# Kernel tuning notes

Hardware: AMD Instinct MI355X
Metric: run time of the kernel (lower is better)

## Reference

```python
import jax, jax.numpy as jnp
import numpy as np

N, D, E, T, R, KMEM, DE = 50000, 128, 800000, 400000, 1, 32, 16
EPS = 1e-5
BETA_MAX = 5.0
GRAD_CLIP = 1.0
STATE_CLIP = 10.0
STEP = 0.1
DAMP = 0.9999  # update_damping=1.0 clamped to 1-1e-4 as in __init__


def segment_logsumexp(s, idx, n):
    # numerically-stable per-segment logsumexp; empty segments contribute 0
    m = jax.ops.segment_max(s, idx, num_segments=n)
    ms = jnp.where(jnp.isfinite(m), m, 0.0)
    z = jax.ops.segment_sum(jnp.exp(s - ms[idx]), idx, num_segments=n)
    return jnp.where(z > 0, jnp.log(jnp.maximum(z, 1e-30)) + ms, 0.0)


def setup_inputs() -> dict:
    key = jax.random.key(0)
    ks = jax.random.split(key, 24)
    inv1 = jnp.log(jnp.expm1(jnp.float32(1.0)))  # _inv_softplus(1.0)
    xav = 0.5 * np.sqrt(2.0 / (2 * D))  # xavier_uniform gain=0.5 ~ std
    inp = {
        'X': jax.random.normal(ks[0], (N, D), jnp.float32),
        'edge_attr': jax.random.normal(ks[1], (E, DE), jnp.float32),
        'ln_gamma': jnp.ones((D,), jnp.float32),
        'ln_beta': jnp.zeros((D,), jnp.float32),
        'W_Q2': jax.random.normal(ks[2], (D, D), jnp.float32) * xav,
        'W_K2': jax.random.normal(ks[3], (D, D), jnp.float32) * xav,
        'W_Q3': jax.random.normal(ks[4], (D, R * D), jnp.float32) * xav,
        'W_K3': jax.random.normal(ks[5], (D, R * D), jnp.float32) * xav,
        'T_tau': jax.random.normal(ks[6], (2, R, D), jnp.float32) * 0.02,
        'W_Qm': jax.random.normal(ks[7], (D, D), jnp.float32) * xav,
        'W_Km': jax.random.normal(ks[8], (D, D), jnp.float32) * xav,
        'B_mem': jax.random.normal(ks[9], (KMEM, D), jnp.float32) / np.sqrt(D),
        'We1': jax.random.normal(ks[10], (DE, D), jnp.float32) / np.sqrt(DE),
        'be1': jnp.zeros((D,), jnp.float32),
        'We2': jax.random.normal(ks[11], (D, 1), jnp.float32) / np.sqrt(D),
        'be2': jnp.zeros((1,), jnp.float32),
        'lambda_2': inv1, 'lambda_3': inv1, 'lambda_m': inv1,
        'beta_2': inv1, 'beta_3': inv1, 'beta_m': inv1,
        'c_2': jax.random.randint(ks[12], (E,), 0, N),
        'u_2': jax.random.randint(ks[13], (E,), 0, N),
        'c_3': jax.random.randint(ks[14], (T,), 0, N),
        'u_3': jax.random.randint(ks[15], (T,), 0, N),
        'v_3': jax.random.randint(ks[16], (T,), 0, N),
        't_tau': jax.random.randint(ks[17], (T,), 0, 2),
    }
    return inp


def reference(X, edge_attr, ln_gamma, ln_beta, W_Q2, W_K2, W_Q3, W_K3, T_tau,
              W_Qm, W_Km, B_mem, We1, be1, We2, be2,
              lambda_2, lambda_3, lambda_m, beta_2, beta_3, beta_m,
              c_2, u_2, c_3, u_3, v_3, t_tau):
    sqrt_d = jnp.sqrt(jnp.float32(D))

    def energy(Xv):
        mu = jnp.mean(Xv, axis=-1, keepdims=True)
        var = jnp.var(Xv, axis=-1, keepdims=True)
        G = (Xv - mu) * jax.lax.rsqrt(var + EPS) * ln_gamma + ln_beta
        # pairwise (order-2) energy over edge list
        b2 = jnp.minimum(jax.nn.softplus(beta_2), BETA_MAX)
        Q2, K2 = G @ W_Q2, G @ W_K2
        a2 = (jax.nn.gelu(edge_attr @ We1 + be1) @ We2 + be2)[:, 0]  # edge_mlp bias
        s2 = b2 * (jnp.sum(Q2[c_2] * K2[u_2], axis=-1) / sqrt_d) + a2  # [E]
        E2 = -(jax.nn.softplus(lambda_2) / b2) * jnp.sum(segment_logsumexp(s2, c_2, N))
        # triplet (order-3) energy with per-type tensor T_tau
        b3 = jnp.minimum(jax.nn.softplus(beta_3), BETA_MAX)
        Q3 = (G @ W_Q3).reshape(-1, R, D)
        K3 = (G @ W_K3).reshape(-1, R, D)
        s3 = b3 * jnp.einsum('erd,erd,erd,erd->e', Q3[c_3], K3[u_3], K3[v_3],
                             T_tau[t_tau]) / jnp.float32(D)  # [T]
        E3 = -(jax.nn.softplus(lambda_3) / b3) * jnp.sum(segment_logsumexp(s3, c_3, N))
        # memory-bank energy
        bm = jnp.minimum(jax.nn.softplus(beta_m), BETA_MAX)
        sm = bm * ((G @ W_Qm) @ (B_mem @ W_Km).T) / sqrt_d  # [N,K]
        Em = -(jax.nn.softplus(lambda_m) / bm) * jnp.sum(jax.nn.logsumexp(sm, axis=1))
        return E2 + E3 + Em

    Eval, gX = jax.value_and_grad(energy)(X)
    gn = jnp.maximum(jnp.linalg.norm(gX, axis=-1, keepdims=True), 1e-6)
    gX = gX * jnp.minimum(GRAD_CLIP / gn, 1.0)
    X_next = X - STEP * DAMP * gX
    sn = jnp.maximum(jnp.linalg.norm(X_next, axis=-1, keepdims=True), 1e-6)
    X_next = X_next * jnp.minimum(STATE_CLIP / sn, 1.0)
    return (X_next, Eval)
```

## Files before the change

### kernel.cpp

```cpp
#include <hip/hip_runtime.h>

#define NN 50000
#define DD 128
#define EE 800000
#define TT 400000
#define KM 32
#define UU 320
#define ROWB 12500
#define MB 782
#define EDGE_BLKS 3125
#define SCAN_TILE 2048
#define SCAN_NB ((NN + SCAN_TILE - 1) / SCAN_TILE)

static constexpr float INV_SQRT_D = 0.08838834764831845f;
static constexpr float INV_D = 1.f / 128.f;

typedef __attribute__((ext_vector_type(8))) short bf16x8;
typedef __attribute__((ext_vector_type(4))) float f32x4;
typedef unsigned short ushort_t;

__device__ __forceinline__ float softplus_f(float x) {
  return (x > 20.f) ? x : log1pf(__expf(x));
}

// ... 226 lines not shown
    __syncthreads();
    *(bf16x8*)&sB[sr][sc * 8] = *(const bf16x8*)(Wc + (size_t)(nb + sr) * 640 + kc * 32 + sc * 8);
    __syncthreads();
    bf16x8 a = *(const bf16x8*)(arp + kc * 32 + quad * 8);
#pragma unroll
    for (int nt = 0; nt < 4; nt++) {
      bf16x8 b = *(const bf16x8*)&sB[nt * 16 + j][quad * 8];
      acc[nt] = __builtin_amdgcn_mfma_f32_16x16x32_bf16(a, b, acc[nt], 0, 0, 0);
    }
  }
#pragma unroll
  for (int nt = 0; nt < 4; nt++)
#pragma unroll
    for (int r = 0; r < 4; r++) {
      int row = row0 + quad * 4 + r;
      if (row < M) ((ushort_t*)dG)[(size_t)row * 128 + nb + nt * 16 + j] = bf16_1(acc[nt][r]);
    }
}

__global__ __launch_bounds__(256, 1) void gemm_km(const float* __restrict__ A,
                                                  const float* __restrict__ W,
                                                  float* __restrict__ C, int M) {
  __shared__ float As[32][132];
  __shared__ float Wst[128][136];
  const int tid = threadIdx.x;
  for (int idx = tid; idx < 128 * 128; idx += 256) {
    int k = idx >> 7, jj = idx & 127;
    Wst[k][jj] = W[k * 128 + jj];
  }
  for (int idx = tid; idx < 32 * 128; idx += 256) {
    int r = idx >> 7, d = idx & 127;
    As[r][d] = A[r * 128 + d];
  }
  __syncthreads();
  int r = tid >> 3, c0 = (tid & 7) * 16;
  float acc[16];
#pragma unroll
  for (int q = 0; q < 16; q++) acc[q] = 0.f;
  for (int k = 0; k < 128; k++) {
    float av = As[r][k];
#pragma unroll
    for (int q = 0; q < 16; q++) acc[q] = fmaf(av, Wst[k][c0 + q], acc[q]);
  }
#pragma unroll
  for (int q = 0; q < 16; q++) C[r * 128 + c0 + q] = acc[q];
}

__global__ __launch_bounds__(256) void hist2(const int* __restrict__ a,
                                             const int* __restrict__ b,
                                             int* __restrict__ ca,
                                             int* __restrict__ cb,
                                             int* __restrict__ pos_a,
                                             int* __restrict__ pos_b, int n) {
  int base = blockIdx.x * 2048 + threadIdx.x;
  if (base + 1792 < n) {
    int av[8], bv[8], pa[8], pb[8];
#pragma unroll
    for (int k = 0; k < 8; k++) { int e = base + k * 256; av[k] = a[e]; bv[k] = b[e]; }
#pragma unroll
    for (int k = 0; k < 8; k++) pa[k] = atomicAdd(&ca[av[k]], 1);
#pragma unroll
    for (int k = 0; k < 8; k++) pb[k] = atomicAdd(&cb[bv[k]], 1);
#pragma unroll
    for (int k = 0; k < 8; k++) pos_a[base + k * 256] = pa[k];
#pragma unroll
    for (int k = 0; k < 8; k++) pos_b[base + k * 256] = pb[k];
  } else {
#pragma unroll
    for (int k = 0; k < 8; k++) {
      int e = base + k * 256;
      if (e < n) {
        pos_a[e] = atomicAdd(&ca[a[e]], 1);
        pos_b[e] = atomicAdd(&cb[b[e]], 1);
      }
    }
  }
}

__global__ __launch_bounds__(256) void hist_t3(const int* __restrict__ c,
                                               const int* __restrict__ u,
                                               const int* __restrict__ v,
                                               int* __restrict__ cc,
                                               int* __restrict__ cuv,
                                               int* __restrict__ pos_c,
                                               int* __restrict__ pos_u,
                                               int* __restrict__ pos_v, int n) {
  int base = blockIdx.x * 2048 + threadIdx.x;
  if (base + 1792 < n) {
    int cv[8], uv[8], vv[8], pc[8], pu[8], pv[8];
#pragma unroll
    for (int k = 0; k < 8; k++) { int t = base + k * 256; cv[k] = c[t]; uv[k] = u[t]; vv[k] = v[t]; }
#pragma unroll
    for (int k = 0; k < 8; k++) pc[k] = atomicAdd(&cc[cv[k]], 1);
#pragma unroll
    for (int k = 0; k < 8; k++) pu[k] = atomicAdd(&cuv[uv[k]], 1);
#pragma unroll
    for (int k = 0; k < 8; k++) pv[k] = atomicAdd(&cuv[vv[k]], 1);
#pragma unroll
    for (int k = 0; k < 8; k++) pos_c[base + k * 256] = pc[k];
#pragma unroll
    for (int k = 0; k < 8; k++) pos_u[base + k * 256] = pu[k];
#pragma unroll
    for (int k = 0; k < 8; k++) pos_v[base + k * 256] = pv[k];
  } else {
#pragma unroll
    for (int k = 0; k < 8; k++) {
      int t = base + k * 256;
      if (t < n) {
        pos_c[t] = atomicAdd(&cc[c[t]], 1);
        pos_u[t] = atomicAdd(&cuv[u[t]], 1);
        pos_v[t] = atomicAdd(&cuv[v[t]], 1);
      }
    }
  }
}

__global__ __launch_bounds__(256) void scan_p1(const int* __restrict__ cnt,
                                               int* __restrict__ part) {
  int arr = blockIdx.y, b = blockIdx.x;
  const int* c = cnt + (size_t)arr * NN;
  int gi = b * SCAN_TILE + threadIdx.x * 8;
  int s = 0;
#pragma unroll
  for (int t = 0; t < 8; t++) s += (gi + t < NN) ? c[gi + t] : 0;
#pragma unroll
  for (int m = 32; m; m >>= 1) s += __shfl_xor(s, m, 64);
  __shared__ int wt[4];
  int lane = threadIdx.x & 63, wid = threadIdx.x >> 6;
  if (lane == 0) wt[wid] = s;
  __syncthreads();
  if (threadIdx.x == 0) part[arr * SCAN_NB + b] = wt[0] + wt[1] + wt[2] + wt[3];
}

__global__ __launch_bounds__(256) void scan_p2(int* __restrict__ part) {
  int w = threadIdx.x >> 6, l = threadIdx.x & 63;
  int v = (l < SCAN_NB) ? part[w * SCAN_NB + l] : 0;
  int x = v;
#pragma unroll
  for (int d = 1; d < 64; d <<= 1) {
    int y = __shfl_up(x, d, 64);
    if (l >= d) x += y;
  }
  if (l < SCAN_NB) part[w * SCAN_NB + l] = x - v;
}

__global__ __launch_bounds__(256) void scan_p3(const int* __restrict__ cnt,
                                               const int* __restrict__ part,
                                               int* __restrict__ rowptr) {
  int arr = blockIdx.y, b = blockIdx.x;
  const int* c = cnt + (size_t)arr * NN;
  int* rp = rowptr + (size_t)arr * (NN + 1);
  int tid = threadIdx.x;
  int gi = b * SCAN_TILE + tid * 8;
  int vals[8];
#pragma unroll
  for (int t = 0; t < 8; t++) vals[t] = (gi + t < NN) ? c[gi + t] : 0;
  int tsum = 0;
#pragma unroll
  for (int t = 0; t < 8; t++) tsum += vals[t];
  int lane = tid & 63, wid = tid >> 6;
  int x = tsum;
#pragma unroll
  for (int d = 1; d < 64; d <<= 1) {
    int y = __shfl_up(x, d, 64);
    if (lane >= d) x += y;
  }
  __shared__ int wt[4];
  if (lane == 63) wt[wid] = x;
  __syncthreads();
  int wadd = 0;
  for (int w = 0; w < wid; w++) wadd += wt[w];
  int running = part[arr * SCAN_NB + b] + wadd + x - tsum;
#pragma unroll
  for (int t = 0; t < 8; t++) {
    if (gi + t < NN) rp[gi + t] = running;
    running += vals[t];
  }
  if (b == SCAN_NB - 1 && tid == 255) rp[NN] = running;
}

__global__ __launch_bounds__(256) void scat2(const int* __restrict__ c2,
                                             const int* __restrict__ u2,
                                             const float* __restrict__ a2,
                                             const int* __restrict__ posc,
                                             const int* __restrict__ posu,
                                             const int* __restrict__ rpc,
                                             const int* __restrict__ rpu,
                                             uint2* __restrict__ payc,
                                             uint2* __restrict__ payu, int n) {
  int base = blockIdx.x * 2048 + threadIdx.x;
  if (base + 1792 < n) {
    int c[8], u[8]; float a[8]; int pc[8], pu[8];
#pragma unroll
    for (int k = 0; k < 8; k++) {
      int e = base + k * 256;
      c[k] = c2[e]; u[k] = u2[e]; a[k] = a2[e]; pc[k] = posc[e]; pu[k] = posu[e];
    }
    int p[8], q[8];
#pragma unroll
    for (int k = 0; k < 8; k++) { p[k] = rpc[c[k]] + pc[k]; q[k] = rpu[u[k]] + pu[k]; }
#pragma unroll
    for (int k = 0; k < 8; k++) {
      uint2 t; t.x = (unsigned)u[k]; t.y = __float_as_uint(a[k]);
      payc[p[k]] = t;
    }
#pragma unroll
    for (int k = 0; k < 8; k++) {
      uint2 t; t.x = (unsigned)p[k]; t.y = (unsigned)c[k];
      payu[q[k]] = t;
    }
  } else {
#pragma unroll
    for (int k = 0; k < 8; k++) {
      int e = base + k * 256;
      if (e < n) {
        int cc = c2[e], uu = u2[e];
        int pp = rpc[cc] + posc[e];
        int qq = rpu[uu] + posu[e];
        uint2 t; t.x = (unsigned)uu; t.y = __float_as_uint(a2[e]);
        payc[pp] = t;
        uint2 t2; t2.x = (unsigned)pp; t2.y = (unsigned)cc;
        payu[qq] = t2;
      }
    }
  }
}

__global__ __launch_bounds__(256) void scat_t3(const int* __restrict__ c3,
                                               const int* __restrict__ u3,
                                               const int* __restrict__ v3,
                                               const int* __restrict__ ttau,
                                               const int* __restrict__ posc,
                                               const int* __restrict__ posu,
                                               const int* __restrict__ posv,
                                               const int* __restrict__ rpc,
                                               const int* __restrict__ rpuv,
                                               uint2* __restrict__ payc,
                                               uint2* __restrict__ payuv, int n) {
  int base = blockIdx.x * 2048 + threadIdx.x;
  if (base + 1792 < n) {
    int c[8], u[8], v[8], ta[8], p[8], q1[8], q2[8];
#pragma unroll
    for (int k = 0; k < 8; k++) {
      int t = base + k * 256;
      c[k] = c3[t]; u[k] = u3[t]; v[k] = v3[t]; ta[k] = ttau[t] & 1;
    }
#pragma unroll
    for (int k = 0; k < 8; k++) {
      int t = base + k * 256;
      p[k] = rpc[c[k]] + posc[t];
      q1[k] = rpuv[u[k]] + posu[t];
      q2[k] = rpuv[v[k]] + posv[t];
    }
#pragma unroll
    for (int k = 0; k < 8; k++) {
      uint2 a; a.x = ((unsigned)u[k] << 16) | (unsigned)v[k]; a.y = (unsigned)ta[k];
      payc[p[k]] = a;
    }
#pragma unroll
    for (int k = 0; k < 8; k++) {
      unsigned sp = ((unsigned)p[k] << 1) | (unsigned)ta[k];
      uint2 b1; b1.x = ((unsigned)v[k] << 16) | (unsigned)c[k]; b1.y = sp;
      payuv[q1[k]] = b1;
      uint2 b2; b2.x = ((unsigned)u[k] << 16) | (unsigned)c[k]; b2.y = sp;
      payuv[q2[k]] = b2;
    }
  } else {
#pragma unroll
    for (int k = 0; k < 8; k++) {
      int t = base + k * 256;
      if (t < n) {
        int c = c3[t], u = u3[t], v = v3[t], ta = ttau[t] & 1;
        int p = rpc[c] + posc[t];
        int q1 = rpuv[u] + posu[t];
        int q2 = rpuv[v] + posv[t];
        unsigned sp = ((unsigned)p << 1) | (unsigned)ta;
        uint2 a; a.x = ((unsigned)u << 16) | (unsigned)v; a.y = (unsigned)ta;
        payc[p] = a;
        uint2 b1; b1.x = ((unsigned)v << 16) | (unsigned)c; b1.y = sp;
        payuv[q1] = b1;
        uint2 b2; b2.x = ((unsigned)u << 16) | (unsigned)c; b2.y = sp;
        payuv[q2] = b2;
      }
    }
  }
}

__device__ void e2_body(int bx, const unsigned* __restrict__ QK,
                        const float* __restrict__ P,
                        const uint2* __restrict__ pay,
                        const int* __restrict__ rp,
                        float* __restrict__ s2c,
                        float* __restrict__ L2,
                        unsigned* __restrict__ dAll) {
  int row = bx * 4 + (threadIdx.x >> 6);
  int l = threadIdx.x & 63, g = l >> 4, j = l & 15;
  float b2s = P[0] * INV_SQRT_D, cw2 = P[3];
  float q[8];
  unp8(*(const uint4*)(QK + (size_t)row * UU + j * 4), q);
  int s = rp[row], e = rp[row + 1];
  float m = -3.0e38f, z = 0.f;
  float acc[8] = {0.f, 0.f, 0.f, 0.f, 0.f, 0.f, 0.f, 0.f};
  int i0 = s + g;
  uint4 kA = {0, 0, 0, 0}, kB = {0, 0, 0, 0};
  float aA = 0.f, aB = 0.f;
  if (i0 < e) {
    uint2 w = pay[i0]; aA = __uint_as_float(w.y);
    kA = *(const uint4*)(QK + (size_t)w.x * UU + 64 + j * 4);
  }
  if (i0 + 4 < e) {
    uint2 w = pay[i0 + 4]; aB = __uint_as_float(w.y);
    kB = *(const uint4*)(QK + (size_t)w.x * UU + 64 + j * 4);
  }
  for (int i = i0; i < e; i += 4) {
    uint4 kC = {0, 0, 0, 0}; float aC = 0.f;
    if (i + 8 < e) {
      uint2 w = pay[i + 8]; aC = __uint_as_float(w.y);
      kC = *(const uint4*)(QK + (size_t)w.x * UU + 64 + j * 4);
    }
    float k[8]; unp8(kA, k);
    float d = 0.f;
#pragma unroll
    for (int t = 0; t < 8; t++) d = fmaf(q[t], k[t], d);
    d = redsum16(d);
    float sv = b2s * d + aA;
    if (j == 0) s2c[i] = sv;
    if (sv <= m) {
      float p = __expf(sv - m);
      z += p;
#pragma unroll
      for (int t = 0; t < 8; t++) acc[t] = fmaf(p, k[t], acc[t]);
    } else {
      float r = __expf(m - sv);
      z = fmaf(z, r, 1.f);
#pragma unroll
      for (int t = 0; t < 8; t++) acc[t] = fmaf(acc[t], r, k[t]);
      m = sv;
    }
    kA = kB; aA = aB; kB = kC; aB = aC;
  }
  float mx = fmaxf(m, __shfl_xor(m, 16, 64));
  mx = fmaxf(mx, __shfl_xor(mx, 32, 64));
  float r = (z > 0.f) ? __expf(m - mx) : 0.f;
  float zz = z * r;
  zz += __shfl_xor(zz, 16, 64);
  zz += __shfl_xor(zz, 32, 64);
#pragma unroll
  for (int t = 0; t < 8; t++) {
    float v = acc[t] * r;
    v += __shfl_xor(v, 16, 64);
    v += __shfl_xor(v, 32, 64);
    acc[t] = v;
  }
  if (l == 0) L2[row] = (zz > 0.f) ? (mx + __logf(zz)) : 0.f;
  if (g == 0) {
    float coef = (zz > 0.f) ? cw2 / zz : 0.f;
    float o[8];
#pragma unroll
    for (int t = 0; t < 8; t++) o[t] = coef * acc[t];
    *(uint4*)(dAll + (size_t)row * UU + 0 + j * 4) = pk8(o);
  }
}

__device__ void t3_body(int bx, const unsigned* __restrict__ QK,
                        const float* __restrict__ Tt,
                        const float* __restrict__ P,
                        const uint2* __restrict__ pay,
                        const int* __restrict__ rp,
                        float* __restrict__ s3c,
                        float* __restrict__ L3,
                        unsigned* __restrict__ dAll) {
  __shared__ float sT[2 * DD];
  int tid = threadIdx.x;
  sT[tid] = Tt[tid];
  __syncthreads();
  int row = bx * 4 + (tid >> 6);
  int l = tid & 63, g = l >> 4, j = l & 15;
  float b3s = P[1] * INV_D, cw3 = P[4];
  float q[8];
  unp8(*(const uint4*)(QK + (size_t)row * UU + 128 + j * 4), q);
  int s = rp[row], e = rp[row + 1];
  float m = -3.0e38f, z = 0.f;
  float acc[8] = {0.f, 0.f, 0.f, 0.f, 0.f, 0.f, 0.f, 0.f};
  int i0 = s + g;
  uint4 kuA = {0, 0, 0, 0}, kvA = {0, 0, 0, 0};
  uint4 kuB = {0, 0, 0, 0}, kvB = {0, 0, 0, 0};
  int taA = 0, taB = 0;
  if (i0 < e) {
    uint2 w = pay[i0]; int u = w.x >> 16, v = w.x & 0xffff; taA = (int)w.y;
    kuA = *(const uint4*)(QK + (size_t)u * UU + 192 + j * 4);
    kvA = *(const uint4*)(QK + (size_t)v * UU + 192 + j * 4);
  }
  if (i0 + 4 < e) {
    uint2 w = pay[i0 + 4]; int u = w.x >> 16, v = w.x & 0xffff; taB = (int)w.y;
    kuB = *(const uint4*)(QK + (size_t)u * UU + 192 + j * 4);
    kvB = *(const uint4*)(QK + (size_t)v * UU + 192 + j * 4);
  }
  for (int i = i0; i < e; i += 4) {
    uint4 kuC = {0, 0, 0, 0}, kvC = {0, 0, 0, 0}; int taC = 0;
    if (i + 8 < e) {
      uint2 w = pay[i + 8]; int u = w.x >> 16, v = w.x & 0xffff; taC = (int)w.y;
      kuC = *(const uint4*)(QK + (size_t)u * UU + 192 + j * 4);
      kvC = *(const uint4*)(QK + (size_t)v * UU + 192 + j * 4);
    }
    float ku[8], kv[8]; unp8(kuA, ku); unp8(kvA, kv);
    const float* tv = &sT[taA * DD + j * 8];
    float et[8], d = 0.f;
#pragma unroll
    for (int t = 0; t < 8; t++) { et[t] = ku[t] * kv[t] * tv[t]; d = fmaf(q[t], et[t], d); }
    d = redsum16(d);
    float sv = b3s * d;
    if (j == 0) s3c[i] = sv;
    if (sv <= m) {
      float p = __expf(sv - m);
      z += p;
#pragma unroll
      for (int t = 0; t < 8; t++) acc[t] = fmaf(p, et[t], acc[t]);
    } else {
      float r = __expf(m - sv);
      z = fmaf(z, r, 1.f);
#pragma unroll
      for (int t = 0; t < 8; t++) acc[t] = fmaf(acc[t], r, et[t]);
      m = sv;
    }
    kuA = kuB; kvA = kvB; taA = taB;
    kuB = kuC; kvB = kvC; taB = taC;
  }
  float mx = fmaxf(m, __shfl_xor(m, 16, 64));
  mx = fmaxf(mx, __shfl_xor(mx, 32, 64));
  float r = (z > 0.f) ? __expf(m - mx) : 0.f;
  float zz = z * r;
  zz += __shfl_xor(zz, 16, 64);
  zz += __shfl_xor(zz, 32, 64);
#pragma unroll
  for (int t = 0; t < 8; t++) {
    float v = acc[t] * r;
    v += __shfl_xor(v, 16, 64);
    v += __shfl_xor(v, 32, 64);
    acc[t] = v;
  }
  if (l == 0) L3[row] = (zz > 0.f) ? (mx + __logf(zz)) : 0.f;
  if (g == 0) {
    float coef = (zz > 0.f) ? cw3 / zz : 0.f;
    float o[8];
#pragma unroll
    for (int t = 0; t < 8; t++) o[t] = coef * acc[t];
    *(uint4*)(dAll + (size_t)row * UU + 128 + j * 4) = pk8(o);
  }
}

__device__ void em_body(int bx, const unsigned* __restrict__ QK,
                        const float* __restrict__ Km,
                        const float* __restrict__ P,
                        unsigned* __restrict__ dAll,
                        float* __restrict__ Lm) {
  __shared__ float sKm[KM * DD];
  int tid = threadIdx.x;
  for (int i = tid; i < KM * DD; i += 256) sKm[i] = Km[i];
  __syncthreads();
  int row = bx * 4 + (tid >> 6);
  int l = tid & 63, g = l >> 4, j = l & 15;
  float bms = P[2] * INV_SQRT_D, cwm = P[5];
  float q[8];
  unp8(*(const uint4*)(QK + (size_t)row * UU + 256 + j * 4), q);
  float dk[8];
#pragma unroll
  for (int kk = 0; kk < 8; kk++) {
    int k = g * 8 + kk;
    const float* kr = &sKm[k * DD + j * 8];
    float d = 0.f;
#pragma unroll
    for (int t = 0; t < 8; t++) d = fmaf(q[t], kr[t], d);
    dk[kk] = redsum16(d) * bms;
  }
  float m = dk[0];
#pragma unroll
  for (int kk = 1; kk < 8; kk++) m = fmaxf(m, dk[kk]);
  float mx = fmaxf(m, __shfl_xor(m, 16, 64));
  mx = fmaxf(mx, __shfl_xor(mx, 32, 64));
  float p[8], z = 0.f;
#pragma unroll
  for (int kk = 0; kk < 8; kk++) { p[kk] = __expf(dk[kk] - mx); z += p[kk]; }
  float zz = z;
  zz += __shfl_xor(zz, 16, 64);
  zz += __shfl_xor(zz, 32, 64);
  if (l == 0) Lm[row] = mx + __logf(zz);
  float coef = cwm / zz;
  float acc[8] = {0.f, 0.f, 0.f, 0.f, 0.f, 0.f, 0.f, 0.f};
#pragma unroll
  for (int kk = 0; kk < 8; kk++) {
    int k = g * 8 + kk;
    const float* kr = &sKm[k * DD + j * 8];
    float pc_ = p[kk] * coef;
#pragma unroll
    for (int t = 0; t < 8; t++) acc[t] = fmaf(pc_, kr[t], acc[t]);
  }
#pragma unroll
  for (int t = 0; t < 8; t++) {
    float v = acc[t];
    v += __shfl_xor(v, 16, 64);
    v += __shfl_xor(v, 32, 64);
    acc[t] = v;
  }
  if (g == 0) *(uint4*)(dAll + (size_t)row * UU + 256 + j * 4) = pk8(acc);
}

__global__ __launch_bounds__(256) void phase2_k(const unsigned* __restrict__ QK,
                                                const float* __restrict__ Tt,
                                                const float* __restrict__ Km,
                                                const float* __restrict__ P,
                                                const uint2* __restrict__ payc2,
                                                const int* __restrict__ rp_c2,
                                                const uint2* __restrict__ payc3,
                                                const int* __restrict__ rp_c3,
                                                float* __restrict__ s2c,
                                                float* __restrict__ L2,
                                                float* __restrict__ s3c,
                                                float* __restrict__ L3,
                                                float* __restrict__ Lm,
                                                unsigned* __restrict__ dAll) {
  int bx = blockIdx.x;
  if (bx < ROWB) e2_body(bx, QK, P, payc2, rp_c2, s2c, L2, dAll);
  else if (bx < 2 * ROWB) t3_body(bx - ROWB, QK, Tt, P, payc3, rp_c3, s3c, L3, dAll);
  else em_body(bx - 2 * ROWB, QK, Km, P, dAll, Lm);
}

__device__ void dk2_body(int bx, const unsigned* __restrict__ QK,
                         const float* __restrict__ s2c,
                         const float* __restrict__ L2,
                         const float* __restrict__ P,
                         const uint2* __restrict__ pay,
                         const int* __restrict__ rp,
                         unsigned* __restrict__ dAll) {
  int row = bx * 4 + (threadIdx.x >> 6);
  int l = threadIdx.x & 63, g = l >> 4, j = l & 15;
  float cw2 = P[3];
  int s = rp[row], e = rp[row + 1];
  float acc[8] = {0.f, 0.f, 0.f, 0.f, 0.f, 0.f, 0.f, 0.f};
  int i0 = s + g;
  uint4 qA = {0, 0, 0, 0}, qB = {0, 0, 0, 0};
  float scA = 0.f, lcA = 0.f, scB = 0.f, lcB = 0.f;
  if (i0 < e) {
    uint2 w = pay[i0]; scA = s2c[w.x]; lcA = L2[w.y];
    qA = *(const uint4*)(QK + (size_t)w.y * UU + 0 + j * 4);
  }
  if (i0 + 4 < e) {
    uint2 w = pay[i0 + 4]; scB = s2c[w.x]; lcB = L2[w.y];
    qB = *(const uint4*)(QK + (size_t)w.y * UU + 0 + j * 4);
  }
  for (int i = i0; i < e; i += 4) {
    uint4 qC = {0, 0, 0, 0}; float scC = 0.f, lcC = 0.f;
    if (i + 8 < e) {
      uint2 w = pay[i + 8]; scC = s2c[w.x]; lcC = L2[w.y];
      qC = *(const uint4*)(QK + (size_t)w.y * UU + 0 + j * 4);
    }
    float w = cw2 * __expf(scA - lcA);
    float qv[8]; unp8(qA, qv);
#pragma unroll
    for (int t = 0; t < 8; t++) acc[t] = fmaf(w, qv[t], acc[t]);
    qA = qB; scA = scB; lcA = lcB;
    qB = qC; scB = scC; lcB = lcC;
  }
#pragma unroll
  for (int t = 0; t < 8; t++) {
    float v = acc[t];
    v += __shfl_xor(v, 16, 64);
    v += __shfl_xor(v, 32, 64);
    acc[t] = v;
  }
  if (g == 0) *(uint4*)(dAll + (size_t)row * UU + 64 + j * 4) = pk8(acc);
}

__device__ void dk3_body(int bx, const unsigned* __restrict__ QK,
                         const float* __restrict__ Tt,
                         const float* __restrict__ s3c,
                         const float* __restrict__ L3,
                         const float* __restrict__ P,
                         const uint2* __restrict__ pay,
                         const int* __restrict__ rp,
                         unsigned* __restrict__ dAll) {
  __shared__ float sT[2 * DD];
  int tid = threadIdx.x;
  sT[tid] = Tt[tid];
  __syncthreads();
  int row = bx * 4 + (tid >> 6);
  int l = tid & 63, g = l >> 4, j = l & 15;
  float cw3 = P[4];
  int s = rp[row], e = rp[row + 1];
  float acc[8] = {0.f, 0.f, 0.f, 0.f, 0.f, 0.f, 0.f, 0.f};
  int i0 = s + g;
  uint4 qA = {0, 0, 0, 0}, kA = {0, 0, 0, 0};
  uint4 qB = {0, 0, 0, 0}, kB = {0, 0, 0, 0};
  int taA = 0, taB = 0;
  float scA = 0.f, lcA = 0.f, scB = 0.f, lcB = 0.f;
  if (i0 < e) {
    uint2 w = pay[i0]; int o = w.x >> 16, c = w.x & 0xffff; unsigned sp = w.y;
    taA = (int)(sp & 1); scA = s3c[sp >> 1]; lcA = L3[c];
    qA = *(const uint4*)(QK + (size_t)c * UU + 128 + j * 4);
    kA = *(const uint4*)(QK + (size_t)o * UU + 192 + j * 4);
  }
  if (i0 + 4 < e) {
    uint2 w = pay[i0 + 4]; int o = w.x >> 16, c = w.x & 0xffff; unsigned sp = w.y;
    taB = (int)(sp & 1); scB = s3c[sp >> 1]; lcB = L3[c];
    qB = *(const uint4*)(QK + (size_t)c * UU + 128 + j * 4);
    kB = *(const uint4*)(QK + (size_t)o * UU + 192 + j * 4);
  }
  for (int i = i0; i < e; i += 4) {
    uint4 qC = {0, 0, 0, 0}, kC = {0, 0, 0, 0}; int taC = 0;
    float scC = 0.f, lcC = 0.f;
    if (i + 8 < e) {
      uint2 w = pay[i + 8]; int o = w.x >> 16, c = w.x & 0xffff; unsigned sp = w.y;
      taC = (int)(sp & 1); scC = s3c[sp >> 1]; lcC = L3[c];
      qC = *(const uint4*)(QK + (size_t)c * UU + 128 + j * 4);
      kC = *(const uint4*)(QK + (size_t)o * UU + 192 + j * 4);
    }
    float w = cw3 * __expf(scA - lcA);
    float qv[8], ko[8]; unp8(qA, qv); unp8(kA, ko);
    const float* tv = &sT[taA * DD + j * 8];
#pragma unroll
    for (int t = 0; t < 8; t++) acc[t] = fmaf(w * tv[t], qv[t] * ko[t], acc[t]);
    qA = qB; kA = kB; taA = taB; scA = scB; lcA = lcB;
    qB = qC; kB = kC; taB = taC; scB = scC; lcB = lcC;
  }
#pragma unroll
  for (int t = 0; t < 8; t++) {
    float v = acc[t];
    v += __shfl_xor(v, 16, 64);
    v += __shfl_xor(v, 32, 64);
    acc[t] = v;
  }
  if (g == 0) *(uint4*)(dAll + (size_t)row * UU + 192 + j * 4) = pk8(acc);
}

__global__ __launch_bounds__(256) void phase3_k(const unsigned* __restrict__ QK,
                                                const float* __restrict__ Tt,
                                                const float* __restrict__ P,
                                                const float* __restrict__ s2c,
                                                const float* __restrict__ L2,
                                                const uint2* __restrict__ payu2,
                                                const int* __restrict__ rp_u2,
                                                const float* __restrict__ s3c,
                                                const float* __restrict__ L3,
                                                const uint2* __restrict__ payuv,
                                                const int* __restrict__ rp_uv,
                                                unsigned* __restrict__ dAll) {
  int bx = blockIdx.x;
  if (bx < ROWB) dk2_body(bx, QK, s2c, L2, P, payu2, rp_u2, dAll);
  else dk3_body(bx - ROWB, QK, Tt, s3c, L3, P, payuv, rp_uv, dAll);
}

__global__ __launch_bounds__(256) void ln_bwd(const float* __restrict__ X,
                                              const unsigned* __restrict__ dG,
                                              const float* __restrict__ gamma,
                                              const float* __restrict__ meanv,
                                              const float* __restrict__ rstdv,
                                              float* __restrict__ out) {
  int row = blockIdx.x * 4 + (threadIdx.x >> 6);
  if (row >= NN) return;
  int l = threadIdx.x & 63;
  float mu = meanv[row], rstd = rstdv[row];
  float2 x2 = *(const float2*)(X + row * DD + 2 * l);
  unsigned gw = dG[(size_t)row * 64 + l];
  float2 ga = *(const float2*)(gamma + 2 * l);
  float xh0 = (x2.x - mu) * rstd, xh1 = (x2.y - mu) * rstd;
  float dh0 = blo(gw) * ga.x, dh1 = bhi(gw) * ga.y;
  float sa = wredsum(dh0 + dh1) * (1.f / DD);
  float sb = wredsum(dh0 * xh0 + dh1 * xh1) * (1.f / DD);
  float dx0 = rstd * (dh0 - sa - xh0 * sb);
  float dx1 = rstd * (dh1 - sa - xh1 * sb);
  float gn = fmaxf(sqrtf(wredsum(dx0 * dx0 + dx1 * dx1)), 1e-6f);
  float sc = fminf(1.f / gn, 1.f);
  dx0 *= sc; dx1 *= sc;
  float xn0 = x2.x - 0.1f * 0.9999f * dx0;
  float xn1 = x2.y - 0.1f * 0.9999f * dx1;
  float sn = fmaxf(sqrtf(wredsum(xn0 * xn0 + xn1 * xn1)), 1e-6f);
  float sc2 = fminf(10.f / sn, 1.f);
  float2 o; o.x = xn0 * sc2; o.y = xn1 * sc2;
  *(float2*)(out + row * DD + 2 * l) = o;
}

__global__ __launch_bounds__(256) void eval_write(const float* __restrict__ L2,
                                                  const float* __restrict__ L3,
                                                  const float* __restrict__ Lm,
                                                  const float* __restrict__ P,
                                                  float* __restrict__ out) {
  int i = blockIdx.x * 256 + threadIdx.x;
  float a2 = 0.f, a3 = 0.f, am = 0.f;
  if (i < NN) { a2 = L2[i]; a3 = L3[i]; am = Lm[i]; }
  a2 = wredsum(a2); a3 = wredsum(a3); am = wredsum(am);
  __shared__ float r2[4], r3[4], rm[4];
  int wv = threadIdx.x >> 6, l = threadIdx.x & 63;
  if (l == 0) { r2[wv] = a2; r3[wv] = a3; rm[wv] = am; }
  __syncthreads();
  if (threadIdx.x == 0) {
    float S2 = r2[0] + r2[1] + r2[2] + r2[3];
    float S3 = r3[0] + r3[1] + r3[2] + r3[3];
    float Sm = rm[0] + rm[1] + rm[2] + rm[3];
    atomicAdd(out, P[6] * S2 + P[7] * S3 + P[8] * Sm);
  }
}

extern "C" void kernel_launch(void* const* d_in, const int* in_sizes, int n_in,
                              void* d_out, int out_size, void* d_ws, size_t ws_size,
                              hipStream_t stream) {
  (void)in_sizes; (void)n_in; (void)out_size;
  const float* X = (const float*)d_in[0];
  const float* EA = (const float*)d_in[1];
  const float* ln_g = (const float*)d_in[2];
  const float* ln_b = (const float*)d_in[3];
  const float* W_Q2 = (const float*)d_in[4];
  const float* W_K2 = (const float*)d_in[5];
  const float* W_Q3 = (const float*)d_in[6];
  const float* W_K3 = (const float*)d_in[7];
  const float* T_tau = (const float*)d_in[8];
  const float* W_Qm = (const float*)d_in[9];
  const float* W_Km = (const float*)d_in[10];
  const float* B_mem = (const float*)d_in[11];
  const float* We1 = (const float*)d_in[12];
  const float* be1 = (const float*)d_in[13];
  const float* We2 = (const float*)d_in[14];
  const float* be2 = (const float*)d_in[15];
  const float* l2s = (const float*)d_in[16];
  const float* l3s = (const float*)d_in[17];
  const float* lms = (const float*)d_in[18];
  const float* b2s = (const float*)d_in[19];
  const float* b3s = (const float*)d_in[20];
  const float* bms = (const float*)d_in[21];
  const int* c2 = (const int*)d_in[22];
  const int* u2 = (const int*)d_in[23];
  const int* c3 = (const int*)d_in[24];
  const int* u3 = (const int*)d_in[25];
  const int* v3 = (const int*)d_in[26];
  const int* ttau = (const int*)d_in[27];
  float* out = (float*)d_out;

  float* ws = (float*)d_ws;
  size_t off = 0;
  auto alloc = [&](size_t n) { float* p = ws + off; off += n; return p; };
  const size_t ND = (size_t)NN * DD;
  unsigned* Gb = (unsigned*)alloc(ND / 2);
  unsigned* QKall = (unsigned*)alloc((size_t)NN * UU);
  unsigned* dAll = (unsigned*)alloc((size_t)NN * UU);
  unsigned* dG = (unsigned*)alloc(ND / 2);
  ushort_t* Wt5 = (ushort_t*)alloc(640 * 128 / 2);
  ushort_t* Wcat = (ushort_t*)alloc(640 * 128 / 2);
  float* Km = alloc((size_t)KM * DD);
  float* a2 = alloc(EE);
  float* s2c = alloc(EE);
  float* s3c = alloc(TT);
  float* meanv = alloc(NN);
  float* rstdv = alloc(NN);
  float* L2 = alloc(NN);
  float* L3 = alloc(NN);
  float* Lm = alloc(NN);
  float* Pparams = alloc(16);
  int* cnt = (int*)alloc(4 * (size_t)NN);
  int* rowptr = (int*)alloc(4 * (size_t)(NN + 1));
  int* spart = (int*)alloc(4 * SCAN_NB);
  int* pos_c2 = (int*)alloc(EE);
  int* pos_u2 = (int*)alloc(EE);
  int* pos_c3 = (int*)alloc(TT);
  int* pos_u3 = (int*)alloc(TT);
  int* pos_v3 = (int*)alloc(TT);
  uint2* payc2 = (uint2*)alloc(2 * (size_t)EE);
  uint2* payu2 = (uint2*)alloc(2 * (size_t)EE);
  uint2* payc3 = (uint2*)alloc(2 * (size_t)TT);
  uint2* payuv = (uint2*)alloc(4 * (size_t)TT);
  if (off * sizeof(float) > ws_size) return;

  int* cnt_c2 = cnt, *cnt_u2 = cnt + NN, *cnt_c3 = cnt + 2 * NN, *cnt_uv = cnt + 3 * NN;
  int* rp_c2 = rowptr, *rp_u2 = rowptr + (NN + 1), *rp_c3 = rowptr + 2 * (NN + 1), *rp_uv = rowptr + 3 * (NN + 1);

  hipMemsetAsync(cnt, 0, 4ull * NN * sizeof(int), stream);
  hipMemsetAsync(out + ND, 0, sizeof(float), stream);

  params_k<<<1, 64, 0, stream>>>(l2s, l3s, lms, b2s, b3s, bms, Pparams);

  int rowB = ROWB;

  ln_fwd<<<rowB, 256, 0, stream>>>(X, ln_g, ln_b, Gb, meanv, rstdv);
  w_conv<<<320, 256, 0, stream>>>(W_Q2, W_K2, W_Q3, W_K3, W_Qm, Wt5, Wcat);
  gemm_km<<<1, 256, 0, stream>>>(B_mem, W_Km, Km, KM);
  fwd_k<<<MB * 10 + EDGE_BLKS, 256, 0, stream>>>((const ushort_t*)Gb, Wt5, (ushort_t*)QKall,
                                                 EA, We1, be1, We2, be2, a2);

  hist2<<<(EE + 2047) / 2048, 256, 0, stream>>>(c2, u2, cnt_c2, cnt_u2, pos_c2, pos_u2, EE);
  hist_t3<<<(TT + 2047) / 2048, 256, 0, stream>>>(c3, u3, v3, cnt_c3, cnt_uv,
                                                  pos_c3, pos_u3, pos_v3, TT);
  scan_p1<<<dim3(SCAN_NB, 4), 256, 0, stream>>>(cnt, spart);
  scan_p2<<<1, 256, 0, stream>>>(spart);
  scan_p3<<<dim3(SCAN_NB, 4), 256, 0, stream>>>(cnt, spart, rowptr);
  scat2<<<(EE + 2047) / 2048, 256, 0, stream>>>(c2, u2, a2, pos_c2, pos_u2,
                                                rp_c2, rp_u2, payc2, payu2, EE);
  scat_t3<<<(TT + 2047) / 2048, 256, 0, stream>>>(c3, u3, v3, ttau,
                                                  pos_c3, pos_u3, pos_v3,
                                                  rp_c3, rp_uv, payc3, payuv, TT);

  phase2_k<<<3 * ROWB, 256, 0, stream>>>(QKall, T_tau, Km, Pparams,
                                         payc2, rp_c2, payc3, rp_c3,
                                         s2c, L2, s3c, L3, Lm, dAll);
  phase3_k<<<2 * ROWB, 256, 0, stream>>>(QKall, T_tau, Pparams,
                                         s2c, L2, payu2, rp_u2,
                                         s3c, L3, payuv, rp_uv, dAll);

  mfma_bwd<<<dim3(MB, 2), 256, 0, stream>>>((const ushort_t*)dAll, Wcat, dG, NN);

  ln_bwd<<<rowB, 256, 0, stream>>>(X, dG, ln_g, meanv, rstdv, out);
  eval_write<<<(NN + 255) / 256, 256, 0, stream>>>(L2, L3, Lm, Pparams, out + ND);
}
```

Measured before the change: 768.3 us.

## Deepen gather prefetch in order-2 edge loops and pad shared tables against bank conflicts

The e2 and dk2 edge loops now process two edges per iteration, with a four-deep register prefetch of gathered key/query rows. This puts more independent global loads in flight to hide gather latency. The T_tau and memory-bank tables move to a single shared buffer declared in the kernel, padded to a stride of 9 floats per 8-element chunk, to cut LDS bank conflicts when lanes read 8-float slices. The cost is higher register pressure and a larger shared allocation for every block, which may lower occupancy.

Measured after the change: 766.9 us. About the same (-0.2%).

```diff
diff --git a/kernel.cpp b/kernel.cpp
--- a/kernel.cpp
+++ b/kernel.cpp
@@ -552,42 +552,60 @@
   float m = -3.0e38f, z = 0.f;
   float acc[8] = {0.f, 0.f, 0.f, 0.f, 0.f, 0.f, 0.f, 0.f};
   int i0 = s + g;
-  uint4 kA = {0, 0, 0, 0}, kB = {0, 0, 0, 0};
-  float aA = 0.f, aB = 0.f;
-  if (i0 < e) {
-    uint2 w = pay[i0]; aA = __uint_as_float(w.y);
-    kA = *(const uint4*)(QK + (size_t)w.x * UU + 64 + j * 4);
-  }
-  if (i0 + 4 < e) {
-    uint2 w = pay[i0 + 4]; aB = __uint_as_float(w.y);
-    kB = *(const uint4*)(QK + (size_t)w.x * UU + 64 + j * 4);
-  }
-  for (int i = i0; i < e; i += 4) {
-    uint4 kC = {0, 0, 0, 0}; float aC = 0.f;
-    if (i + 8 < e) {
-      uint2 w = pay[i + 8]; aC = __uint_as_float(w.y);
-      kC = *(const uint4*)(QK + (size_t)w.x * UU + 64 + j * 4);
-    }
-    float k[8]; unp8(kA, k);
-    float d = 0.f;
-#pragma unroll
-    for (int t = 0; t < 8; t++) d = fmaf(q[t], k[t], d);
-    d = redsum16(d);
-    float sv = b2s * d + aA;
-    if (j == 0) s2c[i] = sv;
-    if (sv <= m) {
-      float p = __expf(sv - m);
-      z += p;
-#pragma unroll
-      for (int t = 0; t < 8; t++) acc[t] = fmaf(p, k[t], acc[t]);
-    } else {
-      float r = __expf(m - sv);
-      z = fmaf(z, r, 1.f);
-#pragma unroll
-      for (int t = 0; t < 8; t++) acc[t] = fmaf(acc[t], r, k[t]);
-      m = sv;
-    }
-    kA = kB; aA = aB; kB = kC; aB = aC;
+  uint4 kA1 = {0,0,0,0}, kA2 = {0,0,0,0}, kB1 = {0,0,0,0}, kB2 = {0,0,0,0};
+  float aA1 = 0.f, aA2 = 0.f, aB1 = 0.f, aB2 = 0.f;
+  if (i0 < e)      { uint2 w = pay[i0];      aA1 = __uint_as_float(w.y); kA1 = *(const uint4*)(QK + (size_t)w.x * UU + 64 + j * 4); }
+  if (i0 + 4 < e)  { uint2 w = pay[i0 + 4];  aA2 = __uint_as_float(w.y); kA2 = *(const uint4*)(QK + (size_t)w.x * UU + 64 + j * 4); }
+  if (i0 + 8 < e)  { uint2 w = pay[i0 + 8];  aB1 = __uint_as_float(w.y); kB1 = *(const uint4*)(QK + (size_t)w.x * UU + 64 + j * 4); }
+  if (i0 + 12 < e) { uint2 w = pay[i0 + 12]; aB2 = __uint_as_float(w.y); kB2 = *(const uint4*)(QK + (size_t)w.x * UU + 64 + j * 4); }
+  for (int i = i0; i < e; i += 8) {
+    uint4 kC1 = {0,0,0,0}, kC2 = {0,0,0,0}; float aC1 = 0.f, aC2 = 0.f;
+    if (i + 16 < e) { uint2 w = pay[i + 16]; aC1 = __uint_as_float(w.y); kC1 = *(const uint4*)(QK + (size_t)w.x * UU + 64 + j * 4); }
+    if (i + 20 < e) { uint2 w = pay[i + 20]; aC2 = __uint_as_float(w.y); kC2 = *(const uint4*)(QK + (size_t)w.x * UU + 64 + j * 4); }
+    {
+      float k[8]; unp8(kA1, k);
+      float d = 0.f;
+#pragma unroll
+      for (int t = 0; t < 8; t++) d = fmaf(q[t], k[t], d);
+      d = redsum16(d);
+      float sv = b2s * d + aA1;
+      if (j == 0) s2c[i] = sv;
+      if (sv <= m) {
+        float p = __expf(sv - m);
+        z += p;
+#pragma unroll
+        for (int t = 0; t < 8; t++) acc[t] = fmaf(p, k[t], acc[t]);
+      } else {
+        float r = __expf(m - sv);
+        z = fmaf(z, r, 1.f);
+#pragma unroll
+        for (int t = 0; t < 8; t++) acc[t] = fmaf(acc[t], r, k[t]);
+        m = sv;
+      }
+    }
+    if (i + 4 < e) {
+      float k[8]; unp8(kA2, k);
+      float d = 0.f;
+#pragma unroll
+      for (int t = 0; t < 8; t++) d = fmaf(q[t], k[t], d);
+      d = redsum16(d);
+      float sv = b2s * d + aA2;
+      if (j == 0) s2c[i + 4] = sv;
+      if (sv <= m) {
+        float p = __expf(sv - m);
+        z += p;
+#pragma unroll
+        for (int t = 0; t < 8; t++) acc[t] = fmaf(p, k[t], acc[t]);
+      } else {
+        float r = __expf(m - sv);
+        z = fmaf(z, r, 1.f);
+#pragma unroll
+        for (int t = 0; t < 8; t++) acc[t] = fmaf(acc[t], r, k[t]);
+        m = sv;
+      }
+    }
+    kA1 = kB1; aA1 = aB1; kA2 = kB2; aA2 = aB2;
+    kB1 = kC1; aB1 = aC1; kB2 = kC2; aB2 = aC2;
   }
   float mx = fmaxf(m, __shfl_xor(m, 16, 64));
   mx = fmaxf(mx, __shfl_xor(mx, 32, 64));
@@ -613,17 +631,14 @@
 }
 
 __device__ void t3_body(int bx, const unsigned* __restrict__ QK,
-                        const float* __restrict__ Tt,
                         const float* __restrict__ P,
                         const uint2* __restrict__ pay,
                         const int* __restrict__ rp,
                         float* __restrict__ s3c,
                         float* __restrict__ L3,
-                        unsigned* __restrict__ dAll) {
-  __shared__ float sT[2 * DD];
+                        unsigned* __restrict__ dAll,
+                        const float* __restrict__ sT) {
   int tid = threadIdx.x;
-  sT[tid] = Tt[tid];
-  __syncthreads();
   int row = bx * 4 + (tid >> 6);
   int l = tid & 63, g = l >> 4, j = l & 15;
   float b3s = P[1] * INV_D, cw3 = P[4];
@@ -633,8 +648,8 @@
   float m = -3.0e38f, z = 0.f;
   float acc[8] = {0.f, 0.f, 0.f, 0.f, 0.f, 0.f, 0.f, 0.f};
   int i0 = s + g;
-  uint4 kuA = {0, 0, 0, 0}, kvA = {0, 0, 0, 0};
-  uint4 kuB = {0, 0, 0, 0}, kvB = {0, 0, 0, 0};
+  uint4 kuA = {0,0,0,0}, kvA = {0,0,0,0};
+  uint4 kuB = {0,0,0,0}, kvB = {0,0,0,0};
   int taA = 0, taB = 0;
   if (i0 < e) {
     uint2 w = pay[i0]; int u = w.x >> 16, v = w.x & 0xffff; taA = (int)w.y;
@@ -647,14 +662,14 @@
     kvB = *(const uint4*)(QK + (size_t)v * UU + 192 + j * 4);
   }
   for (int i = i0; i < e; i += 4) {
-    uint4 kuC = {0, 0, 0, 0}, kvC = {0, 0, 0, 0}; int taC = 0;
+    uint4 kuC = {0,0,0,0}, kvC = {0,0,0,0}; int taC = 0;
     if (i + 8 < e) {
       uint2 w = pay[i + 8]; int u = w.x >> 16, v = w.x & 0xffff; taC = (int)w.y;
       kuC = *(const uint4*)(QK + (size_t)u * UU + 192 + j * 4);
       kvC = *(const uint4*)(QK + (size_t)v * UU + 192 + j * 4);
     }
     float ku[8], kv[8]; unp8(kuA, ku); unp8(kvA, kv);
-    const float* tv = &sT[taA * DD + j * 8];
+    const float* tv = &sT[taA * 144 + j * 9];
     float et[8], d = 0.f;
 #pragma unroll
     for (int t = 0; t < 8; t++) { et[t] = ku[t] * kv[t] * tv[t]; d = fmaf(q[t], et[t], d); }
@@ -700,14 +715,11 @@
 }
 
 __device__ void em_body(int bx, const unsigned* __restrict__ QK,
-                        const float* __restrict__ Km,
                         const float* __restrict__ P,
                         unsigned* __restrict__ dAll,
-                        float* __restrict__ Lm) {
-  __shared__ float sKm[KM * DD];
+                        float* __restrict__ Lm,
+                        const float* __restrict__ sKm) {
   int tid = threadIdx.x;
-  for (int i = tid; i < KM * DD; i += 256) sKm[i] = Km[i];
-  __syncthreads();
   int row = bx * 4 + (tid >> 6);
   int l = tid & 63, g = l >> 4, j = l & 15;
   float bms = P[2] * INV_SQRT_D, cwm = P[5];
@@ -717,7 +729,7 @@
 #pragma unroll
   for (int kk = 0; kk < 8; kk++) {
     int k = g * 8 + kk;
-    const float* kr = &sKm[k * DD + j * 8];
+    const float* kr = &sKm[k * 144 + j * 9];
     float d = 0.f;
 #pragma unroll
     for (int t = 0; t < 8; t++) d = fmaf(q[t], kr[t], d);
@@ -740,7 +752,7 @@
 #pragma unroll
   for (int kk = 0; kk < 8; kk++) {
     int k = g * 8 + kk;
-    const float* kr = &sKm[k * DD + j * 8];
+    const float* kr = &sKm[k * 144 + j * 9];
     float pc_ = p[kk] * coef;
 #pragma unroll
     for (int t = 0; t < 8; t++) acc[t] = fmaf(pc_, kr[t], acc[t]);
@@ -769,10 +781,26 @@
                                                 float* __restrict__ L3,
                                                 float* __restrict__ Lm,
                                                 unsigned* __restrict__ dAll) {
+  __shared__ float smem[32 * 144];
   int bx = blockIdx.x;
-  if (bx < ROWB) e2_body(bx, QK, P, payc2, rp_c2, s2c, L2, dAll);
-  else if (bx < 2 * ROWB) t3_body(bx - ROWB, QK, Tt, P, payc3, rp_c3, s3c, L3, dAll);
-  else em_body(bx - 2 * ROWB, QK, Km, P, dAll, Lm);
+  int tid = threadIdx.x;
+  if (bx < ROWB) {
+    e2_body(bx, QK, P, payc2, rp_c2, s2c, L2, dAll);
+  } else if (bx < 2 * ROWB) {
+    {
+      int ta = tid >> 7, d = tid & 127;
+      smem[ta * 144 + (d >> 3) * 9 + (d & 7)] = Tt[tid];
+    }
+    __syncthreads();
+    t3_body(bx - ROWB, QK, P, payc3, rp_c3, s3c, L3, dAll, smem);
+  } else {
+    for (int i = tid; i < KM * DD; i += 256) {
+      int k = i >> 7, d = i & 127;
+      smem[k * 144 + (d >> 3) * 9 + (d & 7)] = Km[i];
+    }
+    __syncthreads();
+    em_body(bx - 2 * ROWB, QK, P, dAll, Lm, smem);
+  }
 }
 
 __device__ void dk2_body(int bx, const unsigned* __restrict__ QK,
@@ -788,28 +816,32 @@
   int s = rp[row], e = rp[row + 1];
   float acc[8] = {0.f, 0.f, 0.f, 0.f, 0.f, 0.f, 0.f, 0.f};
   int i0 = s + g;
-  uint4 qA = {0, 0, 0, 0}, qB = {0, 0, 0, 0};
-  float scA = 0.f, lcA = 0.f, scB = 0.f, lcB = 0.f;
-  if (i0 < e) {
-    uint2 w = pay[i0]; scA = s2c[w.x]; lcA = L2[w.y];
-    qA = *(const uint4*)(QK + (size_t)w.y * UU + 0 + j * 4);
-  }
-  if (i0 + 4 < e) {
-    uint2 w = pay[i0 + 4]; scB = s2c[w.x]; lcB = L2[w.y];
-    qB = *(const uint4*)(QK + (size_t)w.y * UU + 0 + j * 4);
-  }
-  for (int i = i0; i < e; i += 4) {
-    uint4 qC = {0, 0, 0, 0}; float scC = 0.f, lcC = 0.f;
-    if (i + 8 < e) {
-      uint2 w = pay[i + 8]; scC = s2c[w.x]; lcC = L2[w.y];
-      qC = *(const uint4*)(QK + (size_t)w.y * UU + 0 + j * 4);
-    }
-    float w = cw2 * __expf(scA - lcA);
-    float qv[8]; unp8(qA, qv);
-#pragma unroll
-    for (int t = 0; t < 8; t++) acc[t] = fmaf(w, qv[t], acc[t]);
-    qA = qB; scA = scB; lcA = lcB;
-    qB = qC; scB = scC; lcB = lcC;
+  uint4 qA1 = {0,0,0,0}, qA2 = {0,0,0,0}, qB1 = {0,0,0,0}, qB2 = {0,0,0,0};
+  float scA1 = 0.f, lcA1 = 0.f, scA2 = 0.f, lcA2 = 0.f;
+  float scB1 = 0.f, lcB1 = 0.f, scB2 = 0.f, lcB2 = 0.f;
+  if (i0 < e)      { uint2 w = pay[i0];      scA1 = s2c[w.x]; lcA1 = L2[w.y]; qA1 = *(const uint4*)(QK + (size_t)w.y * UU + 0 + j * 4); }
+  if (i0 + 4 < e)  { uint2 w = pay[i0 + 4];  scA2 = s2c[w.x]; lcA2 = L2[w.y]; qA2 = *(const uint4*)(QK + (size_t)w.y * UU + 0 + j * 4); }
+  if (i0 + 8 < e)  { uint2 w = pay[i0 + 8];  scB1 = s2c[w.x]; lcB1 = L2[w.y]; qB1 = *(const uint4*)(QK + (size_t)w.y * UU + 0 + j * 4); }
+  if (i0 + 12 < e) { uint2 w = pay[i0 + 12]; scB2 = s2c[w.x]; lcB2 = L2[w.y]; qB2 = *(const uint4*)(QK + (size_t)w.y * UU + 0 + j * 4); }
+  for (int i = i0; i < e; i += 8) {
+    uint4 qC1 = {0,0,0,0}, qC2 = {0,0,0,0};
+    float scC1 = 0.f, lcC1 = 0.f, scC2 = 0.f, lcC2 = 0.f;
+    if (i + 16 < e) { uint2 w = pay[i + 16]; scC1 = s2c[w.x]; lcC1 = L2[w.y]; qC1 = *(const uint4*)(QK + (size_t)w.y * UU + 0 + j * 4); }
+    if (i + 20 < e) { uint2 w = pay[i + 20]; scC2 = s2c[w.x]; lcC2 = L2[w.y]; qC2 = *(const uint4*)(QK + (size_t)w.y * UU + 0 + j * 4); }
+    {
+      float w1 = cw2 * __expf(scA1 - lcA1);
+      float qv[8]; unp8(qA1, qv);
+#pragma unroll
+      for (int t = 0; t < 8; t++) acc[t] = fmaf(w1, qv[t], acc[t]);
+    }
+    if (i + 4 < e) {
+      float w2 = cw2 * __expf(scA2 - lcA2);
+      float qv[8]; unp8(qA2, qv);
+#pragma unroll
+      for (int t = 0; t < 8; t++) acc[t] = fmaf(w2, qv[t], acc[t]);
+    }
+    qA1 = qB1; scA1 = scB1; lcA1 = lcB1; qA2 = qB2; scA2 = scB2; lcA2 = lcB2;
+    qB1 = qC1; scB1 = scC1; lcB1 = lcC1; qB2 = qC2; scB2 = scC2; lcB2 = lcC2;
   }
 #pragma unroll
   for (int t = 0; t < 8; t++) {
@@ -822,25 +854,22 @@
 }
 
 __device__ void dk3_body(int bx, const unsigned* __restrict__ QK,
-                         const float* __restrict__ Tt,
                          const float* __restrict__ s3c,
                          const float* __restrict__ L3,
                          const float* __restrict__ P,
                          const uint2* __restrict__ pay,
                          const int* __restrict__ rp,
-                         unsigned* __restrict__ dAll) {
-  __shared__ float sT[2 * DD];
+                         unsigned* __restrict__ dAll,
+                         const float* __restrict__ sT) {
   int tid = threadIdx.x;
-  sT[tid] = Tt[tid];
-  __syncthreads();
   int row = bx * 4 + (tid >> 6);
   int l = tid & 63, g = l >> 4, j = l & 15;
   float cw3 = P[4];
   int s = rp[row], e = rp[row + 1];
   float acc[8] = {0.f, 0.f, 0.f, 0.f, 0.f, 0.f, 0.f, 0.f};
   int i0 = s + g;
-  uint4 qA = {0, 0, 0, 0}, kA = {0, 0, 0, 0};
-  uint4 qB = {0, 0, 0, 0}, kB = {0, 0, 0, 0};
+  uint4 qA = {0,0,0,0}, kA = {0,0,0,0};
+  uint4 qB = {0,0,0,0}, kB = {0,0,0,0};
   int taA = 0, taB = 0;
   float scA = 0.f, lcA = 0.f, scB = 0.f, lcB = 0.f;
   if (i0 < e) {
@@ -856,7 +885,7 @@
     kB = *(const uint4*)(QK + (size_t)o * UU + 192 + j * 4);
   }
   for (int i = i0; i < e; i += 4) {
-    uint4 qC = {0, 0, 0, 0}, kC = {0, 0, 0, 0}; int taC = 0;
+    uint4 qC = {0,0,0,0}, kC = {0,0,0,0}; int taC = 0;
     float scC = 0.f, lcC = 0.f;
     if (i + 8 < e) {
       uint2 w = pay[i + 8]; int o = w.x >> 16, c = w.x & 0xffff; unsigned sp = w.y;
@@ -866,7 +895,7 @@
     }
     float w = cw3 * __expf(scA - lcA);
     float qv[8], ko[8]; unp8(qA, qv); unp8(kA, ko);
-    const float* tv = &sT[taA * DD + j * 8];
+    const float* tv = &sT[taA * 144 + j * 9];
 #pragma unroll
     for (int t = 0; t < 8; t++) acc[t] = fmaf(w * tv[t], qv[t] * ko[t], acc[t]);
     qA = qB; kA = kB; taA = taB; scA = scB; lcA = lcB;
@@ -894,9 +923,19 @@
                                                 const uint2* __restrict__ payuv,
                                                 const int* __restrict__ rp_uv,
                                                 unsigned* __restrict__ dAll) {
+  __shared__ float smem[2 * 144];
   int bx = blockIdx.x;
-  if (bx < ROWB) dk2_body(bx, QK, s2c, L2, P, payu2, rp_u2, dAll);
-  else dk3_body(bx - ROWB, QK, Tt, s3c, L3, P, payuv, rp_uv, dAll);
+  int tid = threadIdx.x;
+  if (bx < ROWB) {
+    dk2_body(bx, QK, s2c, L2, P, payu2, rp_u2, dAll);
+  } else {
+    {
+      int ta = tid >> 7, d = tid & 127;
+      smem[ta * 144 + (d >> 3) * 9 + (d & 7)] = Tt[tid];
+    }
+    __syncthreads();
+    dk3_body(bx - ROWB, QK, s3c, L3, P, payuv, rp_uv, dAll, smem);
+  }
 }
 
 __global__ __launch_bounds__(256) void ln_bwd(const float* __restrict__ X,
```
